# Performance work log

Measured on AMD Instinct MI355X. Metric: run time of the kernel, lower is better.

Reference implementation:

```python
import jax, jax.numpy as jnp
import numpy as np

B, N, E = 2, 2048, 1024
H, D = 16, 64


def setup_inputs() -> dict:
    key = jax.random.key(0)
    k1, k2, k3 = jax.random.split(key, 3)
    x = jax.random.normal(k1, (B, N, E), dtype=jnp.float32)
    Wqkv = jax.random.normal(k2, (3 * H * D, E), dtype=jnp.float32) * 0.02
    bqkv = jnp.zeros((3 * H * D,), dtype=jnp.float32)
    Wout = jax.random.normal(k3, (E, H * D), dtype=jnp.float32) * 0.02
    bout = jnp.zeros((E,), dtype=jnp.float32)
    return {"x": x, "Wqkv": Wqkv, "bqkv": bqkv, "Wout": Wout, "bout": bout}


def reference(x, Wqkv, bqkv, Wout, bout):
    b, n, _ = x.shape
    scale = D ** (-0.5)
    # qkv projection: [b, n, 3*h*d], interpreted as (h, d, qkv) per einops pattern
    qkv = (x @ Wqkv.T + bqkv).reshape(b, n, H, D, 3)
    q = jnp.transpose(qkv[..., 0], (0, 2, 1, 3))  # [b, h, n, d]
    k = jnp.transpose(qkv[..., 1], (0, 2, 1, 3))
    v = jnp.transpose(qkv[..., 2], (0, 2, 1, 3))
    att = jnp.einsum('bhid,bhjd->bhij', q, k) * scale  # [b, h, n, n]
    causal = jnp.tril(jnp.ones((n, n), dtype=bool))
    att = jnp.where(causal, att, -jnp.inf)
    att = jax.nn.softmax(att, axis=-1)
    out = jnp.einsum('bhij,bhjd->bhid', att, v)  # [b, h, n, d]
    out = jnp.transpose(out, (0, 2, 1, 3)).reshape(b, n, H * D)
    return out @ Wout.T + bout
```

## Files before the change

### kernel.cpp

```cpp
#include <hip/hip_runtime.h>
#include <hip/hip_bf16.h>

#define B_ 2
#define N_ 2048
#define E_ 1024
#define H_ 16
#define D_ 64
#define M_ 4096
#define HD_ 1024
#define NT_ 3072

using f32x4  = __attribute__((ext_vector_type(4))) float;
using f32x16 = __attribute__((ext_vector_type(16))) float;
using bf16x8 = __attribute__((ext_vector_type(8))) short;

static __device__ __forceinline__ unsigned short f2bf(float f) {
  union { float f; unsigned u; } v; v.f = f;
  unsigned r = v.u + 0x7FFF + ((v.u >> 16) & 1);
  return (unsigned short)(r >> 16);
}
static __device__ __forceinline__ float bf2f(short s) {
  union { unsigned u; float f; } v; v.u = ((unsigned)(unsigned short)s) << 16; return v.f;
}

static __device__ __forceinline__ void gld16(const void* g, void* l) {
  __builtin_amdgcn_global_load_lds(
      (const __attribute__((address_space(1))) unsigned int*)g,
      (__attribute__((address_space(3))) unsigned int*)l, 16, 0, 0);
}

static __device__ __forceinline__ unsigned cvtpk(float lo, float hi) {
  unsigned r;
  asm("v_cvt_pk_bf16_f32 %0, %1, %2" : "=v"(r) : "v"(lo), "v"(hi));
  return r;
}
static __device__ __forceinline__ void pl32swap(unsigned& a, unsigned& b) {
  asm("v_permlane32_swap_b32 %0, %1" : "+v"(a), "+v"(b));
}

static __device__ __forceinline__ int gswz(int row) {
  return ((row >> 1) & 3) ^ ((row >> 3) & 1);
}

__global__ void k_cvt(const float* __restrict__ x, unsigned short* __restrict__ xb,
                      const float* __restrict__ wq, const float* __restrict__ bsrc,
                      unsigned short* __restrict__ wqb, float* __restrict__ br,
                      const float* __restrict__ wo, unsigned short* __restrict__ wob) {
  int b = blockIdx.x;
  if (b < 4096) {
    int t = b * 256 + threadIdx.x;
    float4 v = reinterpret_cast<const float4*>(x)[t];
    ushort4 o;
    o.x = f2bf(v.x); o.y = f2bf(v.y); o.z = f2bf(v.z); o.w = f2bf(v.w);
    reinterpret_cast<ushort4*>(xb)[t] = o;
  } else if (b < 7168) {
    int t = (b - 4096) * 256 + threadIdx.x;
    int r = t >> 8;
    int c = (t & 255) * 4;
    int kind = r >> 10, hd = r & 1023;
    int h = hd >> 6, d = hd & 63;
    int rin = h * 192 + d * 3 + kind;
    float s = (kind == 0) ? 0.125f * 1.4426950408889634f : 1.0f;
    float4 v = *reinterpret_cast<const float4*>(wq + (size_t)rin * E_ + c);
    ushort4 o;
    o.x = f2bf(v.x * s); o.y = f2bf(v.y * s); o.z = f2bf(v.z * s); o.w = f2bf(v.w * s);
    *reinterpret_cast<ushort4*>(wqb + (size_t)r * E_ + c) = o;
    if (c == 0) br[r] = bsrc[rin] * s;
  } else {
    int t = (b - 7168) * 256 + threadIdx.x;
    int r = t >> 8;
    int c = (t & 255) * 4;
    float4 v = *reinterpret_cast<const float4*>(wo + (size_t)r * HD_ + c);
    ushort4 o;
    o.x = f2bf(v.x); o.y = f2bf(v.y); o.z = f2bf(v.z); o.w = f2bf(v.w);
    *reinterpret_cast<ushort4*>(wob + (size_t)r * HD_ + c) = o;
  }
}

template <int EPI, int BM>
__global__ __launch_bounds__(256, 2) void k_gemm(
    const unsigned short* __restrict__ A,
    const unsigned short* __restrict__ W,
    const float* __restrict__ bias,
    unsigned short* __restrict__ Qo, unsigned short* __restrict__ Ko,
    unsigned short* __restrict__ Vo, float* __restrict__ Fo,
    int M, int Nt, int K)
{
  constexpr int APT = (BM == 128) ? 2 : 1;
  constexpr int LPI = APT + 2;
  constexpr int NF  = (BM == 128) ? 4 : 2;
  constexpr int ASZ = 3 * BM * 32;
  constexpr int MAIN_B = (ASZ + 3 * 128 * 32) * 2;
  constexpr int EPI_B  = (EPI == 0) ? 128 * 136 * 2 : 64 * 132 * 4;
  constexpr int SMB = MAIN_B > EPI_B ? MAIN_B : EPI_B;
  __shared__ alignas(16) char smem[SMB];
  unsigned short* AsBase = (unsigned short*)smem;
  unsigned short* BsBase = AsBase + ASZ;

  const int t = threadIdx.x;
  const int w = t >> 6, l = t & 63, lg = l >> 4, lr = l & 15;
  const int wrow0 = (BM == 128) ? (w >> 1) * 64 : 0;
  const int wcol0 = (BM == 128) ? (w & 1) * 64 : w * 32;
  const int row0 = blockIdx.x * BM, col0 = blockIdx.y * 128;
  const int NT = K >> 5;

  f32x4 acc[4][NF] = {};

  auto stage = [&](int b, int k0) {
#pragma unroll
    for (int c = 0; c < APT; ++c) {
      int ci = w * APT + c;
      int row = ci * 16 + (l >> 2);
      int sub = (l & 3) ^ gswz(row);
      gld16(A + (size_t)(row0 + row) * K + k0 + sub * 8, AsBase + b * BM * 32 + ci * 512);
    }
#pragma unroll
    for (int c = 0; c < 2; ++c) {
      int ci = w * 2 + c;
      int row = ci * 16 + (l >> 2);
      int sub = (l & 3) ^ gswz(row);
      gld16(W + (size_t)(col0 + row) * K + k0 + sub * 8, BsBase + b * 128 * 32 + ci * 512);
    }
  };

  stage(0, 0);
  stage(1, 32);

  for (int kt = 0; kt < NT; ++kt) {
    const int ib = kt % 3;
    if (kt + 2 < NT) stage((kt + 2) % 3, (kt + 2) * 32);
    const int na = NT - 1 - kt;
    if (na >= 2) {
      if constexpr (LPI == 4) asm volatile("s_waitcnt vmcnt(8)" ::: "memory");
      else                    asm volatile("s_waitcnt vmcnt(6)" ::: "memory");
    } else if (na == 1) {
      if constexpr (LPI == 4) asm volatile("s_waitcnt vmcnt(4)" ::: "memory");
      else                    asm volatile("s_waitcnt vmcnt(3)" ::: "memory");
    } else {
      asm volatile("s_waitcnt vmcnt(0)" ::: "memory");
    }
    asm volatile("s_barrier" ::: "memory");

    bf16x8 af[4], bf[NF];
#pragma unroll
    for (int m = 0; m < 4; ++m) {
      int row = wrow0 + m * 16 + lr;
      af[m] = *reinterpret_cast<const bf16x8*>(
          &AsBase[ib * BM * 32 + row * 32 + ((lg ^ gswz(row)) * 8)]);
    }
#pragma unroll
    for (int n = 0; n < NF; ++n) {
      int row = wcol0 + n * 16 + lr;
      bf[n] = *reinterpret_cast<const bf16x8*>(
          &BsBase[ib * 128 * 32 + row * 32 + ((lg ^ gswz(row)) * 8)]);
    }
    __builtin_amdgcn_s_setprio(1);
#pragma unroll
    for (int m = 0; m < 4; ++m)
#pragma unroll
      for (int n = 0; n < NF; ++n)
        acc[m][n] = __builtin_amdgcn_mfma_f32_16x16x32_bf16(af[m], bf[n], acc[m][n], 0, 0, 0);
    __builtin_amdgcn_s_setprio(0);

    asm volatile("s_barrier" ::: "memory");
  }

  if (EPI == 0) {
    const int kind = col0 >> 10;
    if (kind < 2) {
      unsigned short* eb = (unsigned short*)smem;
#pragma unroll
      for (int m = 0; m < 4; ++m)
#pragma unroll
        for (int n = 0; n < NF; ++n) {
          int c = wcol0 + n * 16 + lr;
          float bb = bias[col0 + c];
#pragma unroll
          for (int rr = 0; rr < 4; ++rr)
            eb[(wrow0 + m * 16 + lg * 4 + rr) * 136 + c] = f2bf(acc[m][n][rr] + bb);
        }
      __syncthreads();
      unsigned short* outp = kind ? Ko : Qo;
      int h0 = (col0 & 1023) >> 6;
      int row = t >> 1, cs = (t & 1) * 64;
      int ro = row0 + row;
      int bi = ro >> 11, ni = ro & 2047;
#pragma unroll
      for (int j = 0; j < 8; ++j) {
        int c = cs + j * 8;
        int h = h0 + (c >> 6), d = c & 63;
        bf16x8 v = *reinterpret_cast<const bf16x8*>(&eb[row * 136 + c]);
        *reinterpret_cast<bf16x8*>(
            &outp[((size_t)(bi * H_ + h) * N_ + ni) * D_ + d]) = v;
      }
    } else {
#pragma unroll
      for (int m = 0; m < 4; ++m)
#pragma unroll
        for (int n = 0; n < NF; ++n) {
          int hd = (col0 + wcol0 + n * 16 + lr) & 1023;
          int h = hd >> 6, d = hd & 63;
          float bb = bias[col0 + wcol0 + n * 16 + lr];
          int ro = row0 + wrow0 + m * 16 + lg * 4;
          int bi = ro >> 11, ni = ro & 2047;
          ushort4 pk;
          pk.x = f2bf(acc[m][n][0] + bb);
          pk.y = f2bf(acc[m][n][1] + bb);
          pk.z = f2bf(acc[m][n][2] + bb);
          pk.w = f2bf(acc[m][n][3] + bb);
          *reinterpret_cast<ushort4*>(
              &Vo[((size_t)(bi * H_ + h) * D_ + d) * N_ + ni]) = pk;
        }
    }
  } else {
    float* ef = (float*)smem;
#pragma unroll
    for (int m = 0; m < 4; ++m)
#pragma unroll
      for (int n = 0; n < NF; ++n) {
        int c = wcol0 + n * 16 + lr;
        float bb = bias[col0 + c];
#pragma unroll
        for (int rr = 0; rr < 4; ++rr)
          ef[(m * 16 + lg * 4 + rr) * 132 + c] = acc[m][n][rr] + bb;
      }
    __syncthreads();
    int row = t >> 2, cs = (t & 3) * 32;
#pragma unroll
    for (int j = 0; j < 8; ++j) {
      float4 v = *reinterpret_cast<const float4*>(&ef[row * 132 + cs + j * 4]);
      *reinterpret_cast<float4*>(
          &Fo[(size_t)(row0 + row) * HD_ + col0 + cs + j * 4]) = v;
    }
  }
}

__global__ __launch_bounds__(256, 3) void k_attn(
    const unsigned short* __restrict__ Q,
    const unsigned short* __restrict__ Kg,
    const unsigned short* __restrict__ Vg,
    unsigned short* __restrict__ O,
    unsigned short* __restrict__ Pp,
    float* __restrict__ Pml)
{
  static const int u_qtA[24] = {15,15,15,14,14,14,13,13,13,12,12,12,11,11,11,10,10, 5, 9, 9, 6, 8, 8, 7};
  static const int u_t0A[24] = { 0,12,23, 0,12,23, 0,12,23, 0,12,23, 0,12,23, 0,12, 1, 0,12, 3, 0,12, 5};
  static const int u_teA[24] = {12,23,32,12,23,30,12,23,28,12,23,26,12,23,24,12,22,12,12,20,14,12,18,16};
  static const int u_psA[24] = { 0, 1, 2, 3, 4, 5, 6, 7, 8, 9,10,11,12,13,14,15,16,26,17,18,24,19,20,22};
  static const int u_qtB[24] = {-1,-1, 0,-1,-1, 1,-1,-1, 2,-1,-1, 3,-1,-1, 4,-1, 5,-1,-1, 6,-1,-1, 7,-1};
  static const int u_teB[24] = { 0, 0, 2, 0, 0, 4, 0, 0, 6, 0, 0, 8, 0, 0,10, 0, 1, 0, 0, 3, 0, 0, 5, 0};
  static const int u_psB[24] = { 0, 0,-1, 0, 0,-1, 0, 0,-1, 0, 0,-1, 0, 0,-1, 0,25, 0, 0,23, 0, 0,21, 0};

  __shared__ alignas(16) unsigned short Ks[3][64 * 64];
  __shared__ alignas(16) unsigned short Vs[3][64 * 64];

  const int t = threadIdx.x;
  const int w = t >> 6, l = t & 63;
  const int lq = l & 31;
  const int hi = l >> 5;
  const int bh = blockIdx.x & 31;
  const int u  = blockIdx.x >> 5;

  const unsigned short* Qb = Q  + (size_t)bh * (N_ * D_);
  const unsigned short* Kb = Kg + (size_t)bh * (N_ * D_);
  const unsigned short* Vb = Vg + (size_t)bh * (N_ * D_);

  const int pr  = l >> 3;
  const int pswz = ((l & 7) ^ pr) * 8;
  const unsigned short* KsrcB = Kb + pr * D_ + pswz;
  const unsigned short* VsrcB = Vb + pr * N_ + pswz;
  const int bi = bh >> 4, h = bh & 15;

  auto stage = [&](int b, int kt_) {
    const int kv = kt_ * 64;
#pragma unroll
    for (int c = 0; c < 2; ++c) {
      int cb = w * 2 + c;
      gld16(KsrcB + kv * D_ + cb * 512, (unsigned short*)&Ks[b][0] + cb * 512);
      gld16(VsrcB + kv + cb * 8 * N_,   (unsigned short*)&Vs[b][0] + cb * 512);
    }
  };

  for (int seg = 0; seg < 2; ++seg) {
    const int qt = (seg == 0) ? u_qtA[u] : u_qtB[u];
    if (qt < 0) break;
    const int t0 = (seg == 0) ? u_t0A[u] : 0;
    const int te = (seg == 0) ? u_teA[u] : u_teB[u];
    const int ps = (seg == 0) ? u_psA[u] : u_psB[u];
    const int q0 = qt * 128;
    const int r0w = q0 + w * 32;
    const int rtop = r0w + 31;
    const int tendW = min(te, (rtop >> 6) + 1);

    bf16x8 qf[4];
#pragma unroll
    for (int ks = 0; ks < 4; ++ks)
      qf[ks] = *reinterpret_cast<const bf16x8*>(
          Qb + (size_t)(r0w + lq) * D_ + ks * 16 + hi * 8);

    f32x16 oacc[2] = {};
    float lrun = 0.f;

    stage(0, t0);
    stage(1, t0 + 1);
    asm volatile("s_waitcnt vmcnt(4)" ::: "memory");
    asm volatile("s_barrier" ::: "memory");

    for (int kt = t0; kt < te; ++kt) {
      const int ib = (kt - t0) % 3;
      if (kt + 2 < te) stage((kt - t0 + 2) % 3, kt + 2);
      const int na = te - 1 - kt;
      if (na >= 2)      asm volatile("s_waitcnt vmcnt(8)" ::: "memory");
      else if (na == 1) asm volatile("s_waitcnt vmcnt(4)" ::: "memory");
      else              asm volatile("s_waitcnt vmcnt(0)" ::: "memory");
      asm volatile("s_barrier" ::: "memory");

      if (kt < tendW) {
        const int kv0 = kt * 64;
        bf16x8 kf[2][4], vf[2][4];
#pragma unroll
        for (int ct = 0; ct < 2; ++ct)
#pragma unroll
          for (int ks = 0; ks < 4; ++ks) {
            int row = ct * 32 + lq;
            kf[ct][ks] = *reinterpret_cast<const bf16x8*>(
                &Ks[ib][row * 64 + (((ks * 2 + hi) ^ (lq & 7)) * 8)]);
          }
#pragma unroll
        for (int dt = 0; dt < 2; ++dt)
#pragma unroll
          for (int j = 0; j < 4; ++j) {
            int row = dt * 32 + lq;
            vf[dt][j] = *reinterpret_cast<const bf16x8*>(
                &Vs[ib][row * 64 + (((j * 2 + hi) ^ (lq & 7)) * 8)]);
          }

        f32x16 sct[2];
        __builtin_amdgcn_s_setprio(1);
#pragma unroll
        for (int ct = 0; ct < 2; ++ct) {
          f32x16 z = {};
#pragma unroll
          for (int ks = 0; ks < 4; ++ks)
            z = __builtin_amdgcn_mfma_f32_32x32x16_bf16(kf[ct][ks], qf[ks], z, 0, 0, 0);
          sct[ct] = z;
        }
        __builtin_amdgcn_s_setprio(0);

        if (kv0 + 63 > r0w) {
          int qrow = r0w + lq;
#pragma unroll
          for (int ct = 0; ct < 2; ++ct)
#pragma unroll
            for (int r = 0; r < 16; ++r) {
              int kv = kv0 + ct * 32 + (r & 3) + 8 * (r >> 2) + 4 * hi;
              if (kv > qrow) sct[ct][r] = -1e30f;
            }
        }

        float s16[16];
#pragma unroll
        for (int r = 0; r < 16; ++r) {
          float p0 = exp2f(sct[0][r]);
          float p1 = exp2f(sct[1][r]);
          sct[0][r] = p0; sct[1][r] = p1;
          s16[r] = p0 + p1;
        }
#pragma unroll
        for (int st = 8; st >= 1; st >>= 1)
#pragma unroll
          for (int r = 0; r < 8; ++r)
            if (r < st) s16[r] += s16[r + st];
        lrun += s16[0] + __shfl_xor(s16[0], 32);

        bf16x8 paf[4];
#pragma unroll
        for (int ct = 0; ct < 2; ++ct) {
          unsigned u0 = cvtpk(sct[ct][0],  sct[ct][1]);
          unsigned u1 = cvtpk(sct[ct][2],  sct[ct][3]);
          unsigned u2 = cvtpk(sct[ct][4],  sct[ct][5]);
          unsigned u3 = cvtpk(sct[ct][6],  sct[ct][7]);
          unsigned u4 = cvtpk(sct[ct][8],  sct[ct][9]);
          unsigned u5 = cvtpk(sct[ct][10], sct[ct][11]);
          unsigned u6 = cvtpk(sct[ct][12], sct[ct][13]);
          unsigned u7 = cvtpk(sct[ct][14], sct[ct][15]);
          pl32swap(u0, u2); pl32swap(u1, u3);
          pl32swap(u4, u6); pl32swap(u5, u7);
          union { unsigned uu[4]; bf16x8 v; } c0, c1;
          c0.uu[0] = u0; c0.uu[1] = u1; c0.uu[2] = u2; c0.uu[3] = u3;
          c1.uu[0] = u4; c1.uu[1] = u5; c1.uu[2] = u6; c1.uu[3] = u7;
          paf[ct * 2]     = c0.v;
          paf[ct * 2 + 1] = c1.v;
        }

        __builtin_amdgcn_s_setprio(1);
#pragma unroll
        for (int dt = 0; dt < 2; ++dt)
#pragma unroll
          for (int j = 0; j < 4; ++j)
            oacc[dt] = __builtin_amdgcn_mfma_f32_32x32x16_bf16(paf[j], vf[dt][j], oacc[dt], 0, 0, 0);
        __builtin_amdgcn_s_setprio(0);
      }

      asm volatile("s_barrier" ::: "memory");
    }

    if (ps >= 0) {
      const int slot = bh * 27 + ps;
      unsigned short* pb = Pp + (size_t)slot * 8192;
#pragma unroll
      for (int dt = 0; dt < 2; ++dt) {
        int d = dt * 32 + lq;
#pragma unroll
        for (int g = 0; g < 4; ++g) {
          ushort4 pk;
          pk.x = f2bf(oacc[dt][g * 4 + 0]);
          pk.y = f2bf(oacc[dt][g * 4 + 1]);
          pk.z = f2bf(oacc[dt][g * 4 + 2]);
          pk.w = f2bf(oacc[dt][g * 4 + 3]);
          *reinterpret_cast<ushort4*>(&pb[d * 128 + w * 32 + 8 * g + 4 * hi]) = pk;
        }
      }
      if (l < 32) Pml[(size_t)slot * 128 + w * 32 + l] = lrun;
    } else {
      float inv = 1.0f / lrun;
      float iv[16];
#pragma unroll
      for (int r = 0; r < 16; ++r)
        iv[r] = __shfl(inv, (r & 3) + 8 * (r >> 2) + 4 * hi);
#pragma unroll
      for (int dt = 0; dt < 2; ++dt)
#pragma unroll
        for (int r = 0; r < 16; ++r) {
          int qr = r0w + (r & 3) + 8 * (r >> 2) + 4 * hi;
          int d = dt * 32 + lq;
          O[((size_t)(bi * N_ + qr) * H_ + h) * D_ + d] = f2bf(oacc[dt][r] * iv[r]);
        }
    }
  }
}

__global__ void k_merge(const unsigned short* __restrict__ Pp,
                        const float* __restrict__ Pml,
                        unsigned short* __restrict__ O) {
  int t = blockIdx.x * 256 + threadIdx.x;
  int dseg = t & 7;
  int rloc = (t >> 3) & 127;
  int r = t >> 10;
  int qtj = r % 11;
  int bh  = r / 11;
  int qt = 5 + qtj;
  int nch = (qt >= 11) ? 3 : 2;
  int base = (qt >= 11) ? (15 - qt) * 3 : 25 - (qt - 5) * 2;
  int s0 = bh * 27 + base;
  float lt = 0.f;
  float acc[8] = {};
  for (int c = 0; c < nch; ++c) {
    int s = s0 + c;
    lt += Pml[(size_t)s * 128 + rloc];
    const unsigned short* pp = Pp + (size_t)s * 8192;
#pragma unroll
    for (int j = 0; j < 8; ++j)
      acc[j] += bf2f((short)pp[(dseg * 8 + j) * 128 + rloc]);
  }
  float inv = 1.0f / lt;
  int n = qt * 128 + rloc;
  int bi = bh >> 4, h = bh & 15;
  bf16x8 res;
#pragma unroll
  for (int j = 0; j < 8; ++j) res[j] = (short)f2bf(acc[j] * inv);
  *reinterpret_cast<bf16x8*>(O + ((size_t)(bi * N_ + n) * H_ + h) * D_ + dseg * 8) = res;
}


extern "C" void kernel_launch(void* const* d_in, const int* in_sizes, int n_in,
                              void* d_out, int out_size, void* d_ws, size_t ws_size,
                              hipStream_t stream) {
  const float* x    = (const float*)d_in[0];
  const float* Wqkv = (const float*)d_in[1];
  const float* bqkv = (const float*)d_in[2];
  const float* Wout = (const float*)d_in[3];
  const float* bout = (const float*)d_in[4];
  float* out = (float*)d_out;

  char* ws = (char*)d_ws;
  unsigned short* xb  = (unsigned short*)ws; ws += (size_t)M_ * E_ * 2;
  unsigned short* wqb = (unsigned short*)ws; ws += (size_t)NT_ * E_ * 2;
  float*          bqr = (float*)ws;          ws += 16384;
  unsigned short* wob = (unsigned short*)ws; ws += (size_t)E_ * HD_ * 2;
  unsigned short* Qb  = (unsigned short*)ws; ws += (size_t)M_ * D_ * H_ * 2;
  unsigned short* Kb  = (unsigned short*)ws; ws += (size_t)M_ * D_ * H_ * 2;
  unsigned short* Vb  = (unsigned short*)ws; ws += (size_t)M_ * D_ * H_ * 2;
  unsigned short* ao  = (unsigned short*)ws; ws += (size_t)M_ * HD_ * 2;

  unsigned short* Pp  = xb;
  float*          Pml = (float*)(xb + (size_t)864 * 8192);

  k_cvt<<<8192, 256, 0, stream>>>(x, xb, Wqkv, bqkv, wqb, bqr, Wout, wob);

  k_gemm<0, 128><<<dim3(M_ / 128, NT_ / 128), 256, 0, stream>>>(
      xb, wqb, bqr, Qb, Kb, Vb, nullptr, M_, NT_, E_);

  k_attn<<<768, 256, 0, stream>>>(Qb, Kb, Vb, ao, Pp, Pml);
  k_merge<<<1408, 256, 0, stream>>>(Pp, Pml, ao);

  k_gemm<1, 64><<<dim3(M_ / 64, HD_ / 128), 256, 0, stream>>>(
      ao, wob, bout, nullptr, nullptr, nullptr, out, M_, HD_, E_);
}
```

Measured before the change: 121.0 us.

## Replace QKV projection GEMM with 256x256-tile, 8-wave double-buffered kernel

Adds a dedicated QKV GEMM kernel with 256x256 output tiles, 512 threads, BK=64 double-buffered LDS staging via direct global-to-LDS loads, XOR-swizzled fragments and phased MFMA issue with barriers. The larger tile raises arithmetic intensity and cuts redundant global loads. The grid shrinks to 16x12=192 blocks, which may underfill the CUs. The epilogue drops the LDS-staged vectorized Q/K stores in favor of scalar bf16 scattered stores, which could cost memory efficiency.

New measurement: 150.5 us. +24.4%, slower.

```diff
diff --git a/kernel.cpp b/kernel.cpp
--- a/kernel.cpp
+++ b/kernel.cpp
@@ -77,6 +77,132 @@
   }
 }
 
+__global__ __launch_bounds__(512, 2) void k_gemm0(
+    const unsigned short* __restrict__ A,
+    const unsigned short* __restrict__ W,
+    const float* __restrict__ bias,
+    unsigned short* __restrict__ Qo, unsigned short* __restrict__ Ko,
+    unsigned short* __restrict__ Vo)
+{
+  __shared__ unsigned short As[2][256 * 64];
+  __shared__ unsigned short Bs[2][256 * 64];
+  const int t = threadIdx.x;
+  const int w = t >> 6, l = t & 63, lg = (l >> 4) & 3, lr = l & 15;
+  const int wr = w >> 2, wc = w & 3;
+  const int row0 = blockIdx.x * 256, col0 = blockIdx.y * 256;
+  const int lrow = l >> 3;
+  const int lsub = ((l & 7) ^ (lrow & 7)) * 8;
+  constexpr int NP = 8;
+
+  f32x4 acc[8][4] = {};
+  bf16x8 af[4][2];
+  bf16x8 bfr[2][2][2];
+
+  auto stageA = [&](int b, int k0) {
+#pragma unroll
+    for (int j = 0; j < 4; ++j) {
+      int chunk = j * 8 + w;
+      gld16(A + (size_t)(row0 + chunk * 8 + lrow) * 1024 + k0 + lsub,
+            (unsigned short*)&As[b][0] + chunk * 512);
+    }
+  };
+  auto stageB = [&](int b, int k0) {
+#pragma unroll
+    for (int j = 0; j < 4; ++j) {
+      int chunk = j * 8 + w;
+      gld16(W + (size_t)(col0 + chunk * 8 + lrow) * 1024 + k0 + lsub,
+            (unsigned short*)&Bs[b][0] + chunk * 512);
+    }
+  };
+  auto load_af = [&](int b, int qm) {
+#pragma unroll
+    for (int mf = 0; mf < 4; ++mf)
+#pragma unroll
+      for (int ks = 0; ks < 2; ++ks) {
+        int row = wr * 128 + qm * 64 + mf * 16 + lr;
+        af[mf][ks] = *reinterpret_cast<const bf16x8*>(
+            &As[b][row * 64 + (((ks * 4 + lg) ^ (row & 7)) * 8)]);
+      }
+  };
+  auto load_bf = [&](int b) {
+#pragma unroll
+    for (int qn = 0; qn < 2; ++qn)
+#pragma unroll
+      for (int nf = 0; nf < 2; ++nf)
+#pragma unroll
+        for (int ks = 0; ks < 2; ++ks) {
+          int row = wc * 64 + qn * 32 + nf * 16 + lr;
+          bfr[qn][nf][ks] = *reinterpret_cast<const bf16x8*>(
+              &Bs[b][row * 64 + (((ks * 4 + lg) ^ (row & 7)) * 8)]);
+        }
+  };
+
+#define MMPH(GM0, QN)                                                          \
+  {                                                                            \
+    __builtin_amdgcn_s_barrier();                                              \
+    __builtin_amdgcn_s_setprio(1);                                             \
+    _Pragma("unroll")                                                          \
+    for (int mf = 0; mf < 4; ++mf)                                             \
+      _Pragma("unroll")                                                        \
+      for (int nf = 0; nf < 2; ++nf) {                                         \
+        acc[(GM0) + mf][(QN)*2 + nf] = __builtin_amdgcn_mfma_f32_16x16x32_bf16(\
+            af[mf][0], bfr[QN][nf][0], acc[(GM0) + mf][(QN)*2 + nf], 0, 0, 0); \
+        acc[(GM0) + mf][(QN)*2 + nf] = __builtin_amdgcn_mfma_f32_16x16x32_bf16(\
+            af[mf][1], bfr[QN][nf][1], acc[(GM0) + mf][(QN)*2 + nf], 0, 0, 0); \
+      }                                                                        \
+    __builtin_amdgcn_s_setprio(0);                                             \
+    __builtin_amdgcn_s_barrier();                                              \
+  }
+
+  stageA(0, 0);  stageB(0, 0);
+  stageA(1, 64); stageB(1, 64);
+  asm volatile("s_waitcnt vmcnt(8)" ::: "memory");
+  __syncthreads();
+
+  for (int tt = 0; tt < NP; ++tt) {
+    if (tt > 0) { stageA(1, (2 * tt + 1) * 64); stageB(1, (2 * tt + 1) * 64); }
+    load_af(0, 0); load_bf(0);
+    MMPH(0, 0)
+    MMPH(0, 1)
+    load_af(0, 1);
+    MMPH(4, 1)
+    MMPH(4, 0)
+    asm volatile("s_waitcnt vmcnt(0)" ::: "memory");
+    __builtin_amdgcn_s_barrier();
+    if (tt + 1 < NP) { stageA(0, (2 * tt + 2) * 64); stageB(0, (2 * tt + 2) * 64); }
+    load_af(1, 0); load_bf(1);
+    MMPH(0, 0)
+    MMPH(0, 1)
+    load_af(1, 1);
+    MMPH(4, 1)
+    MMPH(4, 0)
+    asm volatile("s_waitcnt vmcnt(0)" ::: "memory");
+    __builtin_amdgcn_s_barrier();
+  }
+#undef MMPH
+
+  const int kind = col0 >> 10;
+#pragma unroll
+  for (int gm = 0; gm < 8; ++gm) {
+#pragma unroll
+    for (int nf = 0; nf < 4; ++nf) {
+      int col = col0 + wc * 64 + nf * 16 + lr;
+      float bb = bias[col];
+      int hd = col & 1023, h = hd >> 6, d = hd & 63;
+#pragma unroll
+      for (int rr = 0; rr < 4; ++rr) {
+        int ro = row0 + wr * 128 + gm * 16 + lg * 4 + rr;
+        int bi = ro >> 11, ni = ro & 2047;
+        unsigned short bv = f2bf(acc[gm][nf][rr] + bb);
+        size_t bh = (size_t)(bi * H_ + h);
+        if (kind == 0)      Qo[(bh * N_ + ni) * D_ + d] = bv;
+        else if (kind == 1) Ko[(bh * N_ + ni) * D_ + d] = bv;
+        else                Vo[bh * (size_t)(D_ * N_) + (size_t)d * N_ + ni] = bv;
+      }
+    }
+  }
+}
+
 template <int EPI, int BM>
 __global__ __launch_bounds__(256, 2) void k_gemm(
     const unsigned short* __restrict__ A,
@@ -166,52 +292,6 @@
   }
 
   if (EPI == 0) {
-    const int kind = col0 >> 10;
-    if (kind < 2) {
-      unsigned short* eb = (unsigned short*)smem;
-#pragma unroll
-      for (int m = 0; m < 4; ++m)
-#pragma unroll
-        for (int n = 0; n < NF; ++n) {
-          int c = wcol0 + n * 16 + lr;
-          float bb = bias[col0 + c];
-#pragma unroll
-          for (int rr = 0; rr < 4; ++rr)
-            eb[(wrow0 + m * 16 + lg * 4 + rr) * 136 + c] = f2bf(acc[m][n][rr] + bb);
-        }
-      __syncthreads();
-      unsigned short* outp = kind ? Ko : Qo;
-      int h0 = (col0 & 1023) >> 6;
-      int row = t >> 1, cs = (t & 1) * 64;
-      int ro = row0 + row;
-      int bi = ro >> 11, ni = ro & 2047;
-#pragma unroll
-      for (int j = 0; j < 8; ++j) {
-        int c = cs + j * 8;
-        int h = h0 + (c >> 6), d = c & 63;
-        bf16x8 v = *reinterpret_cast<const bf16x8*>(&eb[row * 136 + c]);
-        *reinterpret_cast<bf16x8*>(
-            &outp[((size_t)(bi * H_ + h) * N_ + ni) * D_ + d]) = v;
-      }
-    } else {
-#pragma unroll
-      for (int m = 0; m < 4; ++m)
-#pragma unroll
-        for (int n = 0; n < NF; ++n) {
-          int hd = (col0 + wcol0 + n * 16 + lr) & 1023;
-          int h = hd >> 6, d = hd & 63;
-          float bb = bias[col0 + wcol0 + n * 16 + lr];
-          int ro = row0 + wrow0 + m * 16 + lg * 4;
-          int bi = ro >> 11, ni = ro & 2047;
-          ushort4 pk;
-          pk.x = f2bf(acc[m][n][0] + bb);
-          pk.y = f2bf(acc[m][n][1] + bb);
-          pk.z = f2bf(acc[m][n][2] + bb);
-          pk.w = f2bf(acc[m][n][3] + bb);
-          *reinterpret_cast<ushort4*>(
-              &Vo[((size_t)(bi * H_ + h) * D_ + d) * N_ + ni]) = pk;
-        }
-    }
   } else {
     float* ef = (float*)smem;
 #pragma unroll
@@ -498,8 +578,8 @@
 
   k_cvt<<<8192, 256, 0, stream>>>(x, xb, Wqkv, bqkv, wqb, bqr, Wout, wob);
 
-  k_gemm<0, 128><<<dim3(M_ / 128, NT_ / 128), 256, 0, stream>>>(
-      xb, wqb, bqr, Qb, Kb, Vb, nullptr, M_, NT_, E_);
+  k_gemm0<<<dim3(M_ / 256, NT_ / 256), 512, 0, stream>>>(
+      xb, wqb, bqr, Qb, Kb, Vb);
 
   k_attn<<<768, 256, 0, stream>>>(Qb, Kb, Vb, ao, Pp, Pml);
   k_merge<<<1408, 256, 0, stream>>>(Pp, Pml, ao);
```
